# Optimization experiments

Hardware: AMD Instinct MI355X
Metric: run time of the kernel (lower is better)

Reference implementation:

```python
import jax, jax.numpy as jnp
import numpy as np

BIG, SMALL = 13, 3
NK = 5                       # ceil(BIG / SMALL)
PADDING = SMALL - 1          # 2
EXTRA_PAD = PADDING - SMALL // 2   # 1
G = 2                        # group_in
C_OUT = 96
C_IN = G * C_OUT * NK        # 960
B, H, W = 16, 56, 56


def setup_inputs() -> dict:
    key = jax.random.key(0)
    k1, k2 = jax.random.split(key, 2)
    rng = np.random.default_rng(0)
    mid = BIG // 2
    real_pad = np.array([mid - i * SMALL - PADDING for i in range(NK)], dtype=np.int32)  # [4,1,-2,-5,-8]

    def perm_pads():
        # per output channel, a random permutation of the nk shift offsets
        return np.concatenate([rng.permutation(real_pad) for _ in range(C_OUT)])

    ph = np.stack([perm_pads() for _ in range(G)])  # (G, C_OUT*NK) horizontal shifts
    pv = np.stack([perm_pads() for _ in range(G)])  # (G, C_OUT*NK) vertical shifts
    pad_hv = np.concatenate([ph, pv], axis=0).T.astype(np.int32)  # (C_OUT*NK, 2*G)

    ids = []
    for _ in range(G):
        col = []
        for _ in range(C_OUT):
            arr = -np.ones(NK, dtype=np.int32)
            pos = rng.choice(NK, min(4, NK), replace=False)
            arr[pos] = np.arange(min(4, NK))
            col.append(arr)
        ids.append(np.concatenate(col))
    idx_identit = np.stack(ids).T.astype(np.int32)  # (C_OUT*NK, G)

    x = jax.random.normal(k1, (B, C_IN, H, W), jnp.float32)
    proj_w = jax.random.normal(k2, (C_OUT, C_IN), jnp.float32) * np.float32(1.0 / np.sqrt(C_IN))
    return {
        'x': x,
        'pad_hv': jnp.asarray(pad_hv),
        'idx_identit': jnp.asarray(idx_identit),
        'local_scale': jnp.ones((1, C_IN, 1, 1), jnp.float32),
        'local_bias': jnp.zeros((1, C_IN, 1, 1), jnp.float32),
        'proj_w': proj_w,
        'fuse_alpha': jnp.float32(0.7),
        'b': B, 'hout': H, 'wout': W,
    }


def reference(x, pad_hv, idx_identit, local_scale, local_bias, proj_w, fuse_alpha, b, hout, wout):
    p = EXTRA_PAD
    xp = jnp.pad(x, ((0, 0), (0, 0), (p, p), (p, p)), mode='edge')  # replicate pad
    Bx, Cin, Hp, Wp = xp.shape

    # per-channel shift offsets: channel ic = g*C_OUT*NK + slot, slot = co*NK + k
    ph = pad_hv[:, :G].T.reshape(-1)  # (C_IN,) horizontal (w-axis) shifts
    pv = pad_hv[:, G:].T.reshape(-1)  # (C_IN,) vertical (h-axis) shifts

    def gather_w(xc, s):  # xc: (B, Hp, Wp), s: scalar int shift
        idx = jnp.arange(wout) + p + s
        valid = ((idx >= 0) & (idx < Wp)).astype(xc.dtype)
        return xc[:, p:p + hout, jnp.clip(idx, 0, Wp - 1)] * valid[None, None, :]

    def gather_h(xc, s):
        idx = jnp.arange(hout) + p + s
        valid = ((idx >= 0) & (idx < Hp)).astype(xc.dtype)
        return xc[:, jnp.clip(idx, 0, Hp - 1), p:p + wout] * valid[None, :, None]

    xh = jax.vmap(gather_w, in_axes=(1, 0), out_axes=1)(xp, ph)  # (B, C_IN, hout, wout)
    xv = jax.vmap(gather_h, in_axes=(1, 0), out_axes=1)(xp, pv)
    x1 = xh.reshape(Bx, G, C_OUT, NK, hout, wout).sum((1, 3))    # horizontal-shift group
    x2 = xv.reshape(Bx, G, C_OUT, NK, hout, wout).sum((1, 3))    # vertical-shift group

    id_mask = (idx_identit.T.reshape(-1) >= 0).astype(xp.dtype)  # (C_IN,) identity slots
    x3 = (xp[:, :, p:p + hout, p:p + wout] * id_mask[None, :, None, None])
    x3 = x3.reshape(Bx, G, C_OUT, NK, hout, wout).sum((1, 3))    # identity group

    global_feat = (x1 + x2 + x3) / 3.0

    local = xp * (local_scale + 1e-5) + local_bias
    local = jax.image.resize(local, (Bx, Cin, hout, wout), method='bilinear')  # align_corners=False
    local = jnp.einsum('bchw,oc->bohw', local, proj_w)  # 1x1 conv, no bias

    return fuse_alpha * global_feat + (1.0 - fuse_alpha) * local
```

## Files before the change

kernel.cpp:

```cpp
#include <hip/hip_runtime.h>
#include <hip/hip_bf16.h>
#include <cstdint>
#include <cstddef>

#define B_    16
#define CIN   960
#define HH    56
#define WW_   56
#define GG    2
#define COUT  96
#define NK_   5
#define PIX   3136
#define NCH   30

#define WF_OFF   0
#define BIAS_OFF 61440
#define Y_OFF    61568

typedef __attribute__((ext_vector_type(8))) short bf16x8;
typedef __attribute__((ext_vector_type(4))) float f32x4;

__device__ __forceinline__ short f2b(float f) {
    union { float f; unsigned u; } c; c.f = f;
    unsigned r = (c.u + 0x7FFFu + ((c.u >> 16) & 1u)) >> 16;
    return (short)r;
}
__device__ __forceinline__ float b2f(short s) {
    union { unsigned u; float f; } c;
    c.u = ((unsigned)(unsigned short)s) << 16;
    return c.f;
}

#define GLOAD_LDS16(gp, lp)                                                        \
    __builtin_amdgcn_global_load_lds(                                              \
        (const __attribute__((address_space(1))) unsigned*)(gp),                   \
        (__attribute__((address_space(3))) unsigned*)(lp), 16, 0, 0)

__global__ void prep_wb(const float* __restrict__ pw, const float* __restrict__ sc,
                        short* __restrict__ wf) {
    int idx = blockIdx.x * 256 + threadIdx.x;
    if (idx >= NCH * 6 * 64) return;
    const int lane = idx & 63;
    const int nf   = idx >> 6;
    const int f    = nf % 6;
    const int n    = nf / 6;
    const int o    = f * 16 + (lane & 15);
    const int c0   = n * 32 + (lane >> 4) * 8;
    bf16x8 v;
#pragma unroll
    for (int k = 0; k < 8; ++k)
        v[k] = f2b(pw[o * CIN + c0 + k] * (sc[c0 + k] + 1e-5f));
    *(bf16x8*)((char*)wf + (size_t)n * 8192 + (f * 64 + lane) * 16) = v;
}

__global__ void prep_bias(const float* __restrict__ pw, const float* __restrict__ bi,
                          float* __restrict__ bias) {
    const int o = blockIdx.x;
    const int l = threadIdx.x;
    float s = 0.f;
    for (int c = l; c < CIN; c += 64) s += pw[o * CIN + c] * bi[c];
#pragma unroll
    for (int off = 32; off; off >>= 1) s += __shfl_down(s, off);
    if (l == 0) bias[o] = s;
}

__global__ __launch_bounds__(512)
void conv_mfma(const float* __restrict__ x, const short* __restrict__ wf,
               short* __restrict__ yb) {
    const int tid  = threadIdx.x;
    const int lane = tid & 63;
    const int wv   = tid >> 6;
    const int m    = wv >> 2;
    const int n    = wv & 3;
    const int b    = blockIdx.y;
    const int px0  = blockIdx.x * 64;

    __shared__ __align__(16) char xsb[3 * 8192];
    __shared__ __align__(16) char wlb[2 * 8192];

    const float* xbase = x + (size_t)b * CIN * PIX + px0;
    const char*  wfB   = (const char*)wf;

    const int sch  = wv * 4 + (lane >> 4);
    const int sS   = (wv >> 1) & 3;
    const int soff = (((lane >> 2) & 3) ^ sS) * 16 + (lane & 3) * 4;
    const int wsub = wv * 1024 + lane * 16;

    const int kb    = lane >> 4;
    const int bcol  = (lane & 15) * 4;
    const int bslot = ((n ^ kb) & 3) * 64;
    const int babs  = kb * 2048 + bslot + bcol;
    const int abase = m * 3072 + lane * 16;

    f32x4 acc0 = {0.f, 0.f, 0.f, 0.f};
    f32x4 acc1 = {0.f, 0.f, 0.f, 0.f};
    f32x4 acc2 = {0.f, 0.f, 0.f, 0.f};

#define XDMA(BS, c0)                                                             \
    GLOAD_LDS16(xbase + (size_t)((c0) + sch) * PIX + soff,                       \
                xsb + (BS) * 8192 + wv * 1024);
#define WDMA(N)                                                                  \
    GLOAD_LDS16(wfB + (size_t)(N) * 8192 + wsub,                                 \
                wlb + ((N) & 1) * 8192 + wv * 1024);

    XDMA(0, 0);
    WDMA(0);
    XDMA(1, 32);

#define STEP(n_, XBI, XBS, VM)                                                   \
    {                                                                            \
        asm volatile("s_waitcnt vmcnt(" #VM ")" ::: "memory");                   \
        asm volatile("s_barrier" ::: "memory");                                  \
        bf16x8 bfrag;                                                            \
        _Pragma("unroll")                                                        \
        for (int k = 0; k < 8; ++k)                                              \
            bfrag[k] = f2b(*(const float*)(xsb + (XBI) * 8192 + babs + k * 256));\
        const char* wp_ = wlb + ((n_) & 1) * 8192 + abase;                       \
        const bf16x8 af0 = *(const bf16x8*)(wp_);                                \
        const bf16x8 af1 = *(const bf16x8*)(wp_ + 1024);                         \
        const bf16x8 af2 = *(const bf16x8*)(wp_ + 2048);                         \
        if ((n_) + 1 < NCH) WDMA((n_) + 1);                                      \
        if ((n_) + 2 < NCH) XDMA(XBS, ((n_) + 2) * 32);                          \
        acc0 = __builtin_amdgcn_mfma_f32_16x16x32_bf16(af0, bfrag, acc0, 0,0,0); \
        acc1 = __builtin_amdgcn_mfma_f32_16x16x32_bf16(af1, bfrag, acc1, 0,0,0); \
        acc2 = __builtin_amdgcn_mfma_f32_16x16x32_bf16(af2, bfrag, acc2, 0,0,0); \
    }

#pragma unroll 1
    for (int mm = 0; mm < 9; ++mm) {
        const int n0 = mm * 3;
        STEP(n0 + 0, 0, 2, 1);
        STEP(n0 + 1, 1, 0, 1);
        STEP(n0 + 2, 2, 1, 1);
    }
    STEP(27, 0, 2, 1);
    STEP(28, 1, 0, 1);
    STEP(29, 2, 1, 0);
#undef STEP
#undef WDMA
#undef XDMA

    short* yp = yb + (size_t)b * COUT * PIX + px0 + n * 16 + (lane & 15);
    const int o0 = m * 48 + (lane >> 4) * 4;
#pragma unroll
    for (int r = 0; r < 4; ++r) yp[(size_t)(o0 +      r) * PIX] = f2b(acc0[r]);
#pragma unroll
    for (int r = 0; r < 4; ++r) yp[(size_t)(o0 + 16 + r) * PIX] = f2b(acc1[r]);
#pragma unroll
    for (int r = 0; r < 4; ++r) yp[(size_t)(o0 + 32 + r) * PIX] = f2b(acc2[r]);
}

__device__ __forceinline__ void rweights56(int o, short* idx, float* wt) {
    const float ratio = 58.0f / 56.0f;
    const float kinv  = 56.0f / 58.0f;
    const float sf = ((float)o + 0.5f) * ratio - 0.5f;
    const int f0 = (int)floorf(sf);
    float sum = 0.f;
#pragma unroll
    for (int t = 0; t < 4; ++t) {
        int i = f0 - 1 + t;
        float w = fmaxf(1.0f - fabsf(sf - (float)i) * kinv, 0.0f);
        if (i < 0 || i > 57) w = 0.0f;
        idx[t] = (short)min(HH - 1, max(0, i - 1));
        wt[t] = w;
        sum += w;
    }
    const float inv = 1.0f / sum;
#pragma unroll
    for (int t = 0; t < 4; ++t) wt[t] *= inv;
}

__global__ __launch_bounds__(256)
void finalize(const float* __restrict__ x, const int* __restrict__ pad_hv,
              const int* __restrict__ idt, const short* __restrict__ yb,
              const float* __restrict__ bias, const float* __restrict__ alpha_p,
              float* __restrict__ out) {
    const int bc = blockIdx.x;
    const int co = bc % COUT;
    const int b  = bc / COUT;
    const int t  = threadIdx.x;

    __shared__ float  ylds[PIX];
    __shared__ float4 wt4[56];
    __shared__ short4 id4[56];
    __shared__ int   ish[10], isv[10], ipl[10];
    __shared__ float fid[10];

    if (t < 10) {
        const int g = t / 5;
        const int k = t - g * 5;
        const int slot = co * NK_ + k;
        ish[t] = pad_hv[slot * 4 + g];
        isv[t] = pad_hv[slot * 4 + 2 + g];
        fid[t] = (idt[slot * 2 + g] >= 0) ? 1.f : 0.f;
        ipl[t] = (g * (COUT * NK_) + slot) * PIX;
    }
    if (t < 56) {
        short ii[4]; float ww[4];
        rweights56(t, ii, ww);
        wt4[t] = make_float4(ww[0], ww[1], ww[2], ww[3]);
        id4[t] = make_short4(ii[0], ii[1], ii[2], ii[3]);
    }
    {
        const short* yp = yb + (size_t)bc * PIX;
#pragma unroll 1
        for (int i = t; i < PIX / 4; i += 256) {
            const short4 s4 = *(const short4*)(yp + i * 4);
            *(float4*)(ylds + i * 4) =
                make_float4(b2f(s4.x), b2f(s4.y), b2f(s4.z), b2f(s4.w));
        }
    }
    __syncthreads();

    int   ish_r[10], isv_r[10], ipl_r[10];
    float fid_r[10];
#pragma unroll
    for (int p = 0; p < 10; ++p) {
        ish_r[p] = ish[p]; isv_r[p] = isv[p];
        ipl_r[p] = ipl[p]; fid_r[p] = fid[p];
    }

    const float alpha = alpha_p[0];
    const float ia    = 1.0f - alpha;
    const float bco   = bias[co];
    const float* xb = x + (size_t)b * CIN * PIX;
    float* op = out + (size_t)bc * PIX;

#pragma unroll 1
    for (int px = t; px < PIX; px += 256) {
        const int h = (px * 18725) >> 20;
        const int w = px - h * WW_;
        const int hrow = px - w;

        float accg = 0.f;
#pragma unroll
        for (int p = 0; p < 10; ++p) {
            const float* xc = xb + ipl_r[p];
            const int jw = w + ish_r[p];
            const float mh = (jw >= -1 && jw <= WW_) ? 1.f : 0.f;
            accg += mh * xc[hrow + min(WW_ - 1, max(0, jw))];

            const int iv = h + isv_r[p];
            const float mv = (iv >= -1 && iv <= HH) ? 1.f : 0.f;
            accg += mv * xc[min(HH - 1, max(0, iv)) * WW_ + w];

            accg += fid_r[p] * xc[px];
        }

        const float4 ww4 = wt4[w];
        const short4 iw4 = id4[w];
        const float4 wh4 = wt4[h];
        const short4 ih4 = id4[h];
        float accl = 0.f;
#pragma unroll
        for (int a = 0; a < 4; ++a) {
            const int row = ((const short*)&ih4)[a] * WW_;
            const float* yr = ylds + row;
            float rs;
            rs = ww4.x * yr[iw4.x];
            rs = fmaf(ww4.y, yr[iw4.y], rs);
            rs = fmaf(ww4.z, yr[iw4.z], rs);
            rs = fmaf(ww4.w, yr[iw4.w], rs);
            accl = fmaf(((const float*)&wh4)[a], rs, accl);
        }
        accl += bco;

        op[px] = alpha * accg * (1.0f / 3.0f) + ia * accl;
    }
}

extern "C" void kernel_launch(void* const* d_in, const int* in_sizes, int n_in,
                              void* d_out, int out_size, void* d_ws, size_t ws_size,
                              hipStream_t stream) {
    const float* x      = (const float*)d_in[0];
    const int*   pad_hv = (const int*)d_in[1];
    const int*   idt    = (const int*)d_in[2];
    const float* lsc    = (const float*)d_in[3];
    const float* lbi    = (const float*)d_in[4];
    const float* pw     = (const float*)d_in[5];
    const float* alpha  = (const float*)d_in[6];
    float* out = (float*)d_out;

    float* ws   = (float*)d_ws;
    short* wf   = (short*)(ws + WF_OFF);
    float* bias = ws + BIAS_OFF;
    short* yb   = (short*)(ws + Y_OFF);

    prep_wb<<<(NCH * 6 * 64 + 255) / 256, 256, 0, stream>>>(pw, lsc, wf);
    prep_bias<<<COUT, 64, 0, stream>>>(pw, lbi, bias);
    conv_mfma<<<dim3(PIX / 64, B_), 512, 0, stream>>>(x, wf, yb);
    finalize<<<B_ * COUT, 256, 0, stream>>>(x, pad_hv, idt, yb, bias, alpha, out);
}
```

Measured before the change: 96.89 us.

## Split conv reduction over channels into two halves across grid z

The 1x1 conv GEMM grid is doubled along z. Each block reduces over half of the 960 input channels and writes a partial bf16 result to one of two workspace buffers, and finalize sums the two partials when loading. This raises the block count from 784 to 1568 so more CUs are busy and tail waves are shorter. The cost is an extra partial buffer to write and read, an extra bf16 rounding step, and a shorter per-block pipeline with relatively more prologue overhead.

```diff
diff --git a/kernel.cpp b/kernel.cpp
--- a/kernel.cpp
+++ b/kernel.cpp
@@ -12,10 +12,12 @@
 #define NK_   5
 #define PIX   3136
 #define NCH   30
+#define NCHH  15
 
 #define WF_OFF   0
 #define BIAS_OFF 61440
-#define Y_OFF    61568
+#define Y0_OFF   61568
+#define Y1_OFF   2470016
 
 typedef __attribute__((ext_vector_type(8))) short bf16x8;
 typedef __attribute__((ext_vector_type(4))) float f32x4;
@@ -66,20 +68,21 @@
 
 __global__ __launch_bounds__(512)
 void conv_mfma(const float* __restrict__ x, const short* __restrict__ wf,
-               short* __restrict__ yb) {
+               short* __restrict__ yb0, short* __restrict__ yb1) {
     const int tid  = threadIdx.x;
     const int lane = tid & 63;
     const int wv   = tid >> 6;
     const int m    = wv >> 2;
     const int n    = wv & 3;
     const int b    = blockIdx.y;
+    const int z    = blockIdx.z;
     const int px0  = blockIdx.x * 64;
 
     __shared__ __align__(16) char xsb[3 * 8192];
     __shared__ __align__(16) char wlb[2 * 8192];
 
-    const float* xbase = x + (size_t)b * CIN * PIX + px0;
-    const char*  wfB   = (const char*)wf;
+    const float* xbase = x + (size_t)b * CIN * PIX + (size_t)z * (NCHH * 32) * PIX + px0;
+    const char*  wfB   = (const char*)wf + (size_t)z * NCHH * 8192;
 
     const int sch  = wv * 4 + (lane >> 4);
     const int sS   = (wv >> 1) & 3;
@@ -119,28 +122,29 @@
         const bf16x8 af0 = *(const bf16x8*)(wp_);                                \
         const bf16x8 af1 = *(const bf16x8*)(wp_ + 1024);                         \
         const bf16x8 af2 = *(const bf16x8*)(wp_ + 2048);                         \
-        if ((n_) + 1 < NCH) WDMA((n_) + 1);                                      \
-        if ((n_) + 2 < NCH) XDMA(XBS, ((n_) + 2) * 32);                          \
+        if ((n_) + 1 < NCHH) WDMA((n_) + 1);                                     \
+        if ((n_) + 2 < NCHH) XDMA(XBS, ((n_) + 2) * 32);                         \
         acc0 = __builtin_amdgcn_mfma_f32_16x16x32_bf16(af0, bfrag, acc0, 0,0,0); \
         acc1 = __builtin_amdgcn_mfma_f32_16x16x32_bf16(af1, bfrag, acc1, 0,0,0); \
         acc2 = __builtin_amdgcn_mfma_f32_16x16x32_bf16(af2, bfrag, acc2, 0,0,0); \
     }
 
 #pragma unroll 1
-    for (int mm = 0; mm < 9; ++mm) {
+    for (int mm = 0; mm < 4; ++mm) {
         const int n0 = mm * 3;
         STEP(n0 + 0, 0, 2, 1);
         STEP(n0 + 1, 1, 0, 1);
         STEP(n0 + 2, 2, 1, 1);
     }
-    STEP(27, 0, 2, 1);
-    STEP(28, 1, 0, 1);
-    STEP(29, 2, 1, 0);
+    STEP(12, 0, 2, 1);
+    STEP(13, 1, 0, 1);
+    STEP(14, 2, 1, 0);
 #undef STEP
 #undef WDMA
 #undef XDMA
 
-    short* yp = yb + (size_t)b * COUT * PIX + px0 + n * 16 + (lane & 15);
+    short* ybz = z ? yb1 : yb0;
+    short* yp = ybz + (size_t)b * COUT * PIX + px0 + n * 16 + (lane & 15);
     const int o0 = m * 48 + (lane >> 4) * 4;
 #pragma unroll
     for (int r = 0; r < 4; ++r) yp[(size_t)(o0 +      r) * PIX] = f2b(acc0[r]);
@@ -172,9 +176,9 @@
 
 __global__ __launch_bounds__(256)
 void finalize(const float* __restrict__ x, const int* __restrict__ pad_hv,
-              const int* __restrict__ idt, const short* __restrict__ yb,
-              const float* __restrict__ bias, const float* __restrict__ alpha_p,
-              float* __restrict__ out) {
+              const int* __restrict__ idt, const short* __restrict__ yb0,
+              const short* __restrict__ yb1, const float* __restrict__ bias,
+              const float* __restrict__ alpha_p, float* __restrict__ out) {
     const int bc = blockIdx.x;
     const int co = bc % COUT;
     const int b  = bc / COUT;
@@ -202,12 +206,15 @@
         id4[t] = make_short4(ii[0], ii[1], ii[2], ii[3]);
     }
     {
-        const short* yp = yb + (size_t)bc * PIX;
+        const short* yp0 = yb0 + (size_t)bc * PIX;
+        const short* yp1 = yb1 + (size_t)bc * PIX;
 #pragma unroll 1
         for (int i = t; i < PIX / 4; i += 256) {
-            const short4 s4 = *(const short4*)(yp + i * 4);
+            const short4 a = *(const short4*)(yp0 + i * 4);
+            const short4 c = *(const short4*)(yp1 + i * 4);
             *(float4*)(ylds + i * 4) =
-                make_float4(b2f(s4.x), b2f(s4.y), b2f(s4.z), b2f(s4.w));
+                make_float4(b2f(a.x) + b2f(c.x), b2f(a.y) + b2f(c.y),
+                            b2f(a.z) + b2f(c.z), b2f(a.w) + b2f(c.w));
         }
     }
     __syncthreads();
@@ -284,10 +291,11 @@
     float* ws   = (float*)d_ws;
     short* wf   = (short*)(ws + WF_OFF);
     float* bias = ws + BIAS_OFF;
-    short* yb   = (short*)(ws + Y_OFF);
+    short* yb0  = (short*)(ws + Y0_OFF);
+    short* yb1  = (short*)(ws + Y1_OFF);
 
     prep_wb<<<(NCH * 6 * 64 + 255) / 256, 256, 0, stream>>>(pw, lsc, wf);
     prep_bias<<<COUT, 64, 0, stream>>>(pw, lbi, bias);
-    conv_mfma<<<dim3(PIX / 64, B_), 512, 0, stream>>>(x, wf, yb);
-    finalize<<<B_ * COUT, 256, 0, stream>>>(x, pad_hv, idt, yb, bias, alpha, out);
-}
+    conv_mfma<<<dim3(PIX / 64, B_, 2), 512, 0, stream>>>(x, wf, yb0, yb1);
+    finalize<<<B_ * COUT, 256, 0, stream>>>(x, pad_hv, idt, yb0, yb1, bias, alpha, out);
+}
```

Result: no change. 95.41 us (-1.5%).
